# Optimization experiments

Measured on AMD Instinct MI355X. Metric: run time of the kernel, lower is better.

## Reference

```python
import jax, jax.numpy as jnp
import numpy as np

N = 50000          # nodes
E = 800000         # edges (avg degree 16)
NS = 0.01          # LeakyReLU negative slope
N_CONVS = 3


def setup_inputs() -> dict:
    key = jax.random.key(0)
    ks = jax.random.split(key, 12)
    g = lambda k, s: (jax.random.normal(k, s, dtype=jnp.float32) * 0.05)
    return dict(
        x=jax.random.normal(ks[0], (N, 16), dtype=jnp.float32),
        edge_index=jax.random.randint(ks[1], (2, E), 0, N),
        edge_weight=jax.random.uniform(ks[2], (E, 1), dtype=jnp.float32),
        # prep MLP: Linear(16,64)+LeakyReLU, Linear(64,64)+Tanh
        Wp_in=g(ks[3], (16, 64)), bp_in=jnp.zeros((64,), jnp.float32),
        Wp_h=g(ks[4], (64, 64)), bp_h=jnp.zeros((64,), jnp.float32),
        # per-conv edge projection Linear(edge_dim=1, 64), stacked over 3 convs
        We=g(ks[5], (N_CONVS, 1, 64)), be=jnp.zeros((N_CONVS, 64), jnp.float32),
        # per-conv nn MLP: Linear(64,64)+LeakyReLU, Linear(64,64)+Tanh
        Wm0=g(ks[6], (N_CONVS, 64, 64)), bm0=jnp.zeros((N_CONVS, 64), jnp.float32),
        Wm1=g(ks[7], (N_CONVS, 64, 64)), bm1=jnp.zeros((N_CONVS, 64), jnp.float32),
        # post MLP: Linear(64,64)+LeakyReLU, Linear(64,32)+Tanh
        Wq0=g(ks[8], (64, 64)), bq0=jnp.zeros((64,), jnp.float32),
        Wq1=g(ks[9], (64, 32)), bq1=jnp.zeros((32,), jnp.float32),
    )


def reference(x, edge_index, edge_weight,
              Wp_in, bp_in, Wp_h, bp_h,
              We, be, Wm0, bm0, Wm1, bm1,
              Wq0, bq0, Wq1, bq1):
    lrelu = lambda v: jax.nn.leaky_relu(v, NS)
    # prep MLP (dropout=0 -> no-op)
    h = lrelu(x @ Wp_in + bp_in)
    h = jnp.tanh(h @ Wp_h + bp_h)
    src, dst = edge_index[0], edge_index[1]
    # stacked GINEConv layers (eps=0): out = nn(x + sum_j ReLU(x_j + lin_e(e_ij)))
    for k in range(N_CONVS):
        e = edge_weight @ We[k] + be[k]              # [E,64] edge embedding
        msg = jax.nn.relu(h[src] + e)                # [E,64] gather + fuse
        agg = jax.ops.segment_sum(msg, dst, num_segments=N)  # [N,64] scatter-sum
        z = agg + h                                  # (1+eps)*x with eps=0
        z = lrelu(z @ Wm0[k] + bm0[k])
        h = jnp.tanh(z @ Wm1[k] + bm1[k])
    # post MLP
    z = lrelu(h @ Wq0 + bq0)
    return jnp.tanh(z @ Wq1 + bq1)                   # [N,32]
```

## Files before the change

kernel.cpp:

```cpp
#include <hip/hip_runtime.h>
#include <hip/hip_fp16.h>
#include <math.h>

#define NS 0.01f
#define CAP 48
#define QS (1.f / 65535.f)
#define POISON 0xAAAAAAAAu

__device__ __forceinline__ float lrelu(float v) { return fmaxf(v, NS * v); }

__device__ __forceinline__ unsigned rel_cnt(unsigned raw) {
    return min(raw, raw - POISON);
}

__global__ void __launch_bounds__(512) build_kernel(
    const int* __restrict__ src, const int* __restrict__ dst,
    const float* __restrict__ ew, int* __restrict__ cnt,
    unsigned* __restrict__ bucket, int E, int fillBlocks,
    const float* __restrict__ x,
    const float* __restrict__ Wp_in, const float* __restrict__ bp_in,
    const float* __restrict__ Wp_h,  const float* __restrict__ bp_h,
    __half* __restrict__ h, int N, int prepBlocks,
    const float* __restrict__ Wm0, const float* __restrict__ Wm1,
    const float* __restrict__ Wq0, const float* __restrict__ Wq1,
    float* __restrict__ WT)
{
    __shared__ float zt[64 * 65];
    const int b = (int)blockIdx.x;
    const int t = threadIdx.x;

    if (b < fillBlocks) {
        const int e = b * 512 + t;
        if (e < E) {
            const int d = dst[e];
            const unsigned p = rel_cnt((unsigned)atomicAdd(&cnt[d], 1));
            if (p < CAP) {
                const unsigned q = __float2uint_rn(ew[e] * 65535.f) & 0xffffu;
                bucket[(size_t)d * CAP + p] = ((unsigned)src[e] << 16) | q;
            }
        }
        return;
    }
    if (b < fillBlocks + prepBlocks) {
        const int n0 = (b - fillBlocks) * 64;
        #pragma unroll
        for (int r = 0; r < 2; ++r) {
            const int idx = r * 512 + t;
            const int nl = idx >> 4, i = idx & 15;
            const int n = n0 + nl;
            zt[nl * 65 + i] = (n < N) ? x[(size_t)n * 16 + i] : 0.f;
        }
        __syncthreads();
        const int lane = t & 63;
        const int w = __builtin_amdgcn_readfirstlane(t >> 6);
        float zx[16];
        #pragma unroll
        for (int i = 0; i < 16; ++i) zx[i] = zt[lane * 65 + i];
        float y[8];
        #pragma unroll
        for (int jj = 0; jj < 8; ++jj) {
            const int j = w * 8 + jj;
            float a = bp_in[j];
            #pragma unroll
            for (int i = 0; i < 16; ++i) a = fmaf(zx[i], Wp_in[i * 64 + j], a);
            y[jj] = lrelu(a);
        }
        __syncthreads();
        #pragma unroll
        for (int jj = 0; jj < 8; ++jj) zt[lane * 65 + w * 8 + jj] = y[jj];
        __syncthreads();
        #pragma unroll
        for (int jj = 0; jj < 8; ++jj) y[jj] = bp_h[w * 8 + jj];
        #pragma unroll
        for (int half = 0; half < 2; ++half) {
            float zh[32];
            #pragma unroll
            for (int i = 0; i < 32; ++i) zh[i] = zt[lane * 65 + half * 32 + i];
            #pragma unroll
            for (int jj = 0; jj < 8; ++jj) {
                const int j = w * 8 + jj;
                #pragma unroll
                for (int i = 0; i < 32; ++i)
                    y[jj] = fmaf(zh[i], Wp_h[(half * 32 + i) * 64 + j], y[jj]);
            }
        }
        __syncthreads();
        #pragma unroll
        for (int jj = 0; jj < 8; ++jj) zt[lane * 65 + w * 8 + jj] = tanhf(y[jj]);
        __syncthreads();
        #pragma unroll
        for (int r = 0; r < 8; ++r) {
            const int idx = r * 512 + t;
            const int nl = idx >> 6, i = idx & 63;
            const int n = n0 + nl;
            if (n < N) h[(size_t)n * 64 + i] = __float2half(zt[nl * 65 + i]);
        }
        return;
    }
    const int o = (b - fillBlocks - prepBlocks) * 512 + t;
    if (o >= 30720) return;
    float v;
    int d = o;
    if (d < 12288) {
        const int k = d >> 12, r = d & 4095, j = r >> 6, i = r & 63;
        v = Wm0[k * 4096 + i * 64 + j];
    } else if ((d -= 12288) < 12288) {
        const int k = d >> 12, r = d & 4095, j = r >> 6, i = r & 63;
        v = Wm1[k * 4096 + i * 64 + j];
    } else if ((d -= 12288) < 4096) {
        const int j = d >> 6, i = d & 63;
        v = Wq0[i * 64 + j];
    } else {
        d -= 4096;
        const int j = d >> 6, i = d & 63;
        v = Wq1[i * 32 + j];
    }
    WT[o] = v;
}

__device__ __forceinline__ void drain_edges(float& acc, int p, int len,
    const unsigned* row,
    const __half* __restrict__ hin, int lane, float wej, float bej)
{
    if (p + 4 <= len) {
        const uint4 a = ((const uint4*)row)[p >> 2];
        const unsigned r[4] = {a.x, a.y, a.z, a.w};
        float g[4];
        #pragma unroll
        for (int q = 0; q < 4; ++q) g[q] = __half2float(hin[(size_t)(r[q] >> 16) * 64 + lane]);
        #pragma unroll
        for (int q = 0; q < 4; ++q)
            acc += fmaxf(g[q] + fmaf((float)(r[q] & 0xffffu) * QS, wej, bej), 0.f);
        p += 4;
    }
    for (; p < len; ++p) {
        const unsigned r = row[p];
        acc += fmaxf(__half2float(hin[(size_t)(r >> 16) * 64 + lane])
                     + fmaf((float)(r & 0xffffu) * QS, wej, bej), 0.f);
    }
}

__device__ __forceinline__ void layer64s(float* zt, int lane, int w,
                                         const float* __restrict__ WT,
                                         const float* __restrict__ bias, int act)
{
    float y[4];
    #pragma unroll
    for (int jj = 0; jj < 4; ++jj) y[jj] = bias[w * 4 + jj];
    #pragma unroll
    for (int half = 0; half < 2; ++half) {
        float zh[32];
        #pragma unroll
        for (int i = 0; i < 32; ++i) zh[i] = zt[lane * 65 + half * 32 + i];
        #pragma unroll
        for (int jj = 0; jj < 4; ++jj) {
            const float* wr = WT + (w * 4 + jj) * 64 + half * 32;
            #pragma unroll
            for (int i = 0; i < 32; ++i) y[jj] = fmaf(zh[i], wr[i], y[jj]);
        }
    }
    __syncthreads();
    #pragma unroll
    for (int jj = 0; jj < 4; ++jj)
        zt[lane * 65 + w * 4 + jj] = act ? lrelu(y[jj]) : tanhf(y[jj]);
    __syncthreads();
}

__global__ void __launch_bounds__(1024, 8) fused_conv_kernel(
    const __half* __restrict__ hin,
    const int* __restrict__ cnt,
    const unsigned* __restrict__ bucket,
    const float* __restrict__ We_k, const float* __restrict__ be_k,
    const float* __restrict__ W0T, const float* __restrict__ b0,
    const float* __restrict__ W1T, const float* __restrict__ b1,
    const float* __restrict__ Wq0T, const float* __restrict__ bq0,
    const float* __restrict__ Wq1T, const float* __restrict__ bq1,
    int do_post, __half* __restrict__ hout, float* __restrict__ out, int N)
{
    __shared__ float zt[64 * 65];
    const int t = threadIdx.x;
    const int lane = t & 63;
    const int w = __builtin_amdgcn_readfirstlane(t >> 6);
    const int n0 = (int)blockIdx.x * 64;
    const float wej = We_k[lane], bej = be_k[lane];

    float acc[4];
    int   len[4];
    const unsigned* row[4];
    #pragma unroll
    for (int s = 0; s < 4; ++s) {
        const int n = n0 + w * 4 + s;
        if (n < N) {
            acc[s] = __half2float(hin[(size_t)n * 64 + lane]);
            len[s] = (int)min(rel_cnt((unsigned)cnt[n]), (unsigned)CAP);
        } else { acc[s] = 0.f; len[s] = 0; }
        row[s] = bucket + (size_t)n * CAP;
    }
    const int maxLen = max(max(len[0], len[1]), max(len[2], len[3]));
    for (int p = 0; p + 8 <= maxLen; p += 8) {
        #pragma unroll
        for (int s = 0; s < 4; ++s) {
            if (p + 8 <= len[s]) {
                const uint4* r4 = (const uint4*)row[s];
                const uint4 a0 = r4[p >> 2], a1 = r4[(p >> 2) + 1];
                const unsigned rr[8] = {a0.x, a0.y, a0.z, a0.w, a1.x, a1.y, a1.z, a1.w};
                float g[8];
                #pragma unroll
                for (int q = 0; q < 8; ++q)
                    g[q] = __half2float(hin[(size_t)(rr[q] >> 16) * 64 + lane]);
                #pragma unroll
                for (int q = 0; q < 8; ++q)
                    acc[s] += fmaxf(g[q] + fmaf((float)(rr[q] & 0xffffu) * QS, wej, bej), 0.f);
            }
        }
    }
    #pragma unroll
    for (int s = 0; s < 4; ++s) {
        drain_edges(acc[s], len[s] & ~7, len[s], row[s], hin, lane, wej, bej);
        zt[(w * 4 + s) * 65 + lane] = acc[s];
    }
    __syncthreads();

    layer64s(zt, lane, w, W0T, b0, 1);
    layer64s(zt, lane, w, W1T, b1, 0);

    if (!do_post) {
        #pragma unroll
        for (int r = 0; r < 4; ++r) {
            const int idx = r * 1024 + t;
            const int nl = idx >> 6, i = idx & 63;
            const int n = n0 + nl;
            if (n < N) hout[(size_t)n * 64 + i] = __float2half(zt[nl * 65 + i]);
        }
        return;
    }
    layer64s(zt, lane, w, Wq0T, bq0, 1);
    {
        float y[2];
        #pragma unroll
        for (int jj = 0; jj < 2; ++jj) y[jj] = bq1[w * 2 + jj];
        #pragma unroll
        for (int half = 0; half < 2; ++half) {
            float zh[32];
            #pragma unroll
            for (int i = 0; i < 32; ++i) zh[i] = zt[lane * 65 + half * 32 + i];
            #pragma unroll
            for (int jj = 0; jj < 2; ++jj) {
                const float* wr = Wq1T + (w * 2 + jj) * 64 + half * 32;
                #pragma unroll
                for (int i = 0; i < 32; ++i) y[jj] = fmaf(zh[i], wr[i], y[jj]);
            }
        }
        __syncthreads();
        #pragma unroll
        for (int jj = 0; jj < 2; ++jj) zt[lane * 65 + w * 2 + jj] = tanhf(y[jj]);
        __syncthreads();
    }
    #pragma unroll
    for (int r = 0; r < 2; ++r) {
        const int idx = r * 1024 + t;
        const int nl = idx >> 5, i = idx & 31;
        const int n = n0 + nl;
        if (n < N) out[(size_t)n * 32 + i] = zt[nl * 65 + i];
    }
}

extern "C" void kernel_launch(void* const* d_in, const int* in_sizes, int n_in,
                              void* d_out, int out_size, void* d_ws, size_t ws_size,
                              hipStream_t stream) {
    const float* x     = (const float*)d_in[0];
    const int*   ei    = (const int*)d_in[1];
    const float* ew    = (const float*)d_in[2];
    const float* Wp_in = (const float*)d_in[3];
    const float* bp_in = (const float*)d_in[4];
    const float* Wp_h  = (const float*)d_in[5];
    const float* bp_h  = (const float*)d_in[6];
    const float* We    = (const float*)d_in[7];
    const float* be    = (const float*)d_in[8];
    const float* Wm0   = (const float*)d_in[9];
    const float* bm0   = (const float*)d_in[10];
    const float* Wm1   = (const float*)d_in[11];
    const float* bm1   = (const float*)d_in[12];
    const float* Wq0   = (const float*)d_in[13];
    const float* bq0   = (const float*)d_in[14];
    const float* Wq1   = (const float*)d_in[15];
    const float* bq1   = (const float*)d_in[16];
    float* out = (float*)d_out;

    const int N = in_sizes[0] / 16;
    const int E = in_sizes[2];
    const int* src = ei;
    const int* dst = ei + E;

    __half*   hA     = (__half*)d_ws;
    __half*   hB     = hA + (size_t)N * 64;
    unsigned* bucket = (unsigned*)(hB + (size_t)N * 64);
    int*      cnt    = (int*)(bucket + (size_t)N * CAP);
    float*    WT     = (float*)(cnt + N);
    float* Wm0T   = WT;
    float* Wm1T   = Wm0T + 12288;
    float* Wq0T   = Wm1T + 12288;
    float* Wq1T   = Wq0T + 4096;

    const int fillBlocks = (E + 511) / 512;
    const int prepBlocks = (N + 63) / 64;
    const int wtBlocks   = (30720 + 511) / 512;
    const int tileBlocks = (N + 63) / 64;

    build_kernel<<<fillBlocks + prepBlocks + wtBlocks, 512, 0, stream>>>(
        src, dst, ew, cnt, bucket, E, fillBlocks,
        x, Wp_in, bp_in, Wp_h, bp_h, hA, N, prepBlocks,
        Wm0, Wm1, Wq0, Wq1, WT);

    fused_conv_kernel<<<tileBlocks, 1024, 0, stream>>>(
        hA, cnt, bucket, We + 0 * 64, be + 0 * 64,
        Wm0T + 0 * 4096, bm0 + 0 * 64, Wm1T + 0 * 4096, bm1 + 0 * 64,
        Wq0T, bq0, Wq1T, bq1, 0, hB, out, N);
    fused_conv_kernel<<<tileBlocks, 1024, 0, stream>>>(
        hB, cnt, bucket, We + 1 * 64, be + 1 * 64,
        Wm0T + 1 * 4096, bm0 + 1 * 64, Wm1T + 1 * 4096, bm1 + 1 * 64,
        Wq0T, bq0, Wq1T, bq1, 0, hA, out, N);
    fused_conv_kernel<<<tileBlocks, 1024, 0, stream>>>(
        hA, cnt, bucket, We + 2 * 64, be + 2 * 64,
        Wm0T + 2 * 4096, bm0 + 2 * 64, Wm1T + 2 * 4096, bm1 + 2 * 64,
        Wq0T, bq0, Wq1T, bq1, 1, hB, out, N);
}
```

Measured before the change: 295.3 us.

## Batch masked neighbor gathers across node pairs and vectorize edge bucket build

The conv aggregation loop now handles two nodes per step, issuing 16 neighbor-row gathers at once and masking out entries past each node's length. This replaces the separate full-chunk loop and the scalar tail drain, so more loads are in flight and there is less branching. The build kernel now processes four edges per thread using vector loads and nontemporal bucket stores, with a quarter as many fill blocks. In exchange, the gather loop reads stale or poisoned bucket slots and does wasted gathers for short rows, and each build thread now does four serialized atomics.

```diff
diff --git a/kernel.cpp b/kernel.cpp
--- a/kernel.cpp
+++ b/kernel.cpp
@@ -30,13 +30,34 @@
     const int t = threadIdx.x;
 
     if (b < fillBlocks) {
-        const int e = b * 512 + t;
-        if (e < E) {
-            const int d = dst[e];
-            const unsigned p = rel_cnt((unsigned)atomicAdd(&cnt[d], 1));
-            if (p < CAP) {
-                const unsigned q = __float2uint_rn(ew[e] * 65535.f) & 0xffffu;
-                bucket[(size_t)d * CAP + p] = ((unsigned)src[e] << 16) | q;
+        const int e0 = (b * 512 + t) * 4;
+        if (e0 + 3 < E && (E & 3) == 0) {
+            const int4   d4 = *(const int4*)(dst + e0);
+            const int4   s4 = *(const int4*)(src + e0);
+            const float4 w4 = *(const float4*)(ew + e0);
+            const int   dd[4] = {d4.x, d4.y, d4.z, d4.w};
+            const int   ss[4] = {s4.x, s4.y, s4.z, s4.w};
+            const float ww[4] = {w4.x, w4.y, w4.z, w4.w};
+            unsigned p[4];
+            #pragma unroll
+            for (int q = 0; q < 4; ++q)
+                p[q] = rel_cnt((unsigned)atomicAdd(&cnt[dd[q]], 1));
+            #pragma unroll
+            for (int q = 0; q < 4; ++q) {
+                if (p[q] < CAP) {
+                    const unsigned qq = __float2uint_rn(ww[q] * 65535.f) & 0xffffu;
+                    __builtin_nontemporal_store(((unsigned)ss[q] << 16) | qq,
+                                                &bucket[(size_t)dd[q] * CAP + p[q]]);
+                }
+            }
+        } else {
+            for (int e = e0; e < min(e0 + 4, E); ++e) {
+                const int d = dst[e];
+                const unsigned p = rel_cnt((unsigned)atomicAdd(&cnt[d], 1));
+                if (p < CAP) {
+                    const unsigned q = __float2uint_rn(ew[e] * 65535.f) & 0xffffu;
+                    bucket[(size_t)d * CAP + p] = ((unsigned)src[e] << 16) | q;
+                }
             }
         }
         return;
@@ -118,28 +139,6 @@
     WT[o] = v;
 }
 
-__device__ __forceinline__ void drain_edges(float& acc, int p, int len,
-    const unsigned* row,
-    const __half* __restrict__ hin, int lane, float wej, float bej)
-{
-    if (p + 4 <= len) {
-        const uint4 a = ((const uint4*)row)[p >> 2];
-        const unsigned r[4] = {a.x, a.y, a.z, a.w};
-        float g[4];
-        #pragma unroll
-        for (int q = 0; q < 4; ++q) g[q] = __half2float(hin[(size_t)(r[q] >> 16) * 64 + lane]);
-        #pragma unroll
-        for (int q = 0; q < 4; ++q)
-            acc += fmaxf(g[q] + fmaf((float)(r[q] & 0xffffu) * QS, wej, bej), 0.f);
-        p += 4;
-    }
-    for (; p < len; ++p) {
-        const unsigned r = row[p];
-        acc += fmaxf(__half2float(hin[(size_t)(r >> 16) * 64 + lane])
-                     + fmaf((float)(r & 0xffffu) * QS, wej, bej), 0.f);
-    }
-}
-
 __device__ __forceinline__ void layer64s(float* zt, int lane, int w,
                                          const float* __restrict__ WT,
                                          const float* __restrict__ bias, int act)
@@ -186,39 +185,56 @@
 
     float acc[4];
     int   len[4];
-    const unsigned* row[4];
+    const uint4* r4[4];
     #pragma unroll
     for (int s = 0; s < 4; ++s) {
         const int n = n0 + w * 4 + s;
+        const int nc = min(n, N - 1);
+        r4[s] = (const uint4*)(bucket + (size_t)nc * CAP);
         if (n < N) {
             acc[s] = __half2float(hin[(size_t)n * 64 + lane]);
             len[s] = (int)min(rel_cnt((unsigned)cnt[n]), (unsigned)CAP);
         } else { acc[s] = 0.f; len[s] = 0; }
-        row[s] = bucket + (size_t)n * CAP;
-    }
-    const int maxLen = max(max(len[0], len[1]), max(len[2], len[3]));
-    for (int p = 0; p + 8 <= maxLen; p += 8) {
-        #pragma unroll
-        for (int s = 0; s < 4; ++s) {
-            if (p + 8 <= len[s]) {
-                const uint4* r4 = (const uint4*)row[s];
-                const uint4 a0 = r4[p >> 2], a1 = r4[(p >> 2) + 1];
-                const unsigned rr[8] = {a0.x, a0.y, a0.z, a0.w, a1.x, a1.y, a1.z, a1.w};
-                float g[8];
-                #pragma unroll
-                for (int q = 0; q < 8; ++q)
-                    g[q] = __half2float(hin[(size_t)(rr[q] >> 16) * 64 + lane]);
-                #pragma unroll
-                for (int q = 0; q < 8; ++q)
-                    acc[s] += fmaxf(g[q] + fmaf((float)(rr[q] & 0xffffu) * QS, wej, bej), 0.f);
-            }
-        }
-    }
-    #pragma unroll
-    for (int s = 0; s < 4; ++s) {
-        drain_edges(acc[s], len[s] & ~7, len[s], row[s], hin, lane, wej, bej);
+    }
+    const int m01 = max(len[0], len[1]);
+    const int m23 = max(len[2], len[3]);
+    const int maxLen = max(m01, m23);
+    for (int p = 0; p < maxLen; p += 8) {
+        #pragma unroll
+        for (int pr = 0; pr < 2; ++pr) {
+            const int mpr = pr ? m23 : m01;
+            if (p < mpr) {
+                const int s0 = pr * 2;
+                unsigned rc[16];
+                #pragma unroll
+                for (int ss = 0; ss < 2; ++ss) {
+                    const uint4 a0 = r4[s0 + ss][p >> 2];
+                    const uint4 a1 = r4[s0 + ss][(p >> 2) + 1];
+                    rc[ss * 8 + 0] = a0.x; rc[ss * 8 + 1] = a0.y;
+                    rc[ss * 8 + 2] = a0.z; rc[ss * 8 + 3] = a0.w;
+                    rc[ss * 8 + 4] = a1.x; rc[ss * 8 + 5] = a1.y;
+                    rc[ss * 8 + 6] = a1.z; rc[ss * 8 + 7] = a1.w;
+                }
+                float g[16];
+                #pragma unroll
+                for (int i = 0; i < 16; ++i)
+                    g[i] = __half2float(hin[(size_t)(rc[i] >> 16) * 64 + lane]);
+                #pragma unroll
+                for (int ss = 0; ss < 2; ++ss) {
+                    const int s = s0 + ss;
+                    #pragma unroll
+                    for (int q = 0; q < 8; ++q) {
+                        const float v = fmaxf(g[ss * 8 + q]
+                            + fmaf((float)(rc[ss * 8 + q] & 0xffffu) * QS, wej, bej), 0.f);
+                        acc[s] += (p + q < len[s]) ? v : 0.f;
+                    }
+                }
+            }
+        }
+    }
+    #pragma unroll
+    for (int s = 0; s < 4; ++s)
         zt[(w * 4 + s) * 65 + lane] = acc[s];
-    }
     __syncthreads();
 
     layer64s(zt, lane, w, W0T, b0, 1);
@@ -302,7 +318,7 @@
     float* Wq0T   = Wm1T + 12288;
     float* Wq1T   = Wq0T + 4096;
 
-    const int fillBlocks = (E + 511) / 512;
+    const int fillBlocks = (E + 2047) / 2048;
     const int prepBlocks = (N + 63) / 64;
     const int wtBlocks   = (30720 + 511) / 512;
     const int tileBlocks = (N + 63) / 64;
```

Result: no change. 297.6 us (+0.8%).
